# Kernel tuning notes

Hardware: AMD Instinct MI355X
Metric: run time of the kernel (lower is better)

Reference implementation:

```python
import jax, jax.numpy as jnp
import numpy as np

N = 2708
IN_C = 1433
OUT_C = 64


def setup_inputs() -> dict:
    key = jax.random.key(0)
    k1, k2, k3, k4, k5, k6, k7 = jax.random.split(key, 7)
    X = jax.random.normal(k1, (N, IN_C), dtype=jnp.float32)
    A = jax.random.randint(k2, (N, N), 0, 2, dtype=jnp.int32)  # dense binary adjacency mask
    # Graph Fourier basis: orthonormal-ish random matrix (QR of gaussian)
    U = jnp.linalg.qr(jax.random.normal(k3, (N, N), dtype=jnp.float32))[0]
    s = 1.0 / np.sqrt(IN_C)
    W_K = jax.random.normal(k4, (OUT_C, IN_C), dtype=jnp.float32) * s
    W_Q = jax.random.normal(k5, (OUT_C, IN_C), dtype=jnp.float32) * s
    W_V = jax.random.normal(k6, (OUT_C, IN_C), dtype=jnp.float32) * s
    lmbd = jax.random.uniform(k7, (N, 1), dtype=jnp.float32)
    return {"X": X, "A": A, "U": U, "W_K": W_K, "W_Q": W_Q, "W_V": W_V, "lmbd": lmbd}


def reference(X, A, U, W_K, W_Q, W_V, lmbd):
    # Linear projections (torch nn.Linear: x @ W.T)
    K = X @ W_K.T  # [N, d]
    Q = X @ W_Q.T  # [N, d]
    V = X @ W_V.T  # [N, d]
    d_k = K.shape[-1]
    E = (Q @ K.T) / d_k  # [N, N]
    # spectral filtering: igft(lmbd * gft(E)) = U @ (lmbd * (U^T @ E))
    E = jnp.abs(U @ (lmbd * (U.T @ E)))
    # masked softmax over neighbors; dropout p=0 in eval mode (no-op)
    E_masked = jnp.where(A == 0, -jnp.inf, E)
    alpha = jax.nn.softmax(E_masked, axis=-1)
    H = alpha @ V  # [N, d]
    return H
```

## Files before the change

kernel.cpp:

```cpp
#include <hip/hip_runtime.h>

#define NV 2708
#define INC 1433
#define XCOLS 1472
#define UDIM 2752
#define PSTR 2720
#define BSTR 2752
#define SLAB ((size_t)(2752*64))
#define MWPR 88

typedef __attribute__((ext_vector_type(8))) short bf16x8;
typedef __attribute__((ext_vector_type(4))) float f32x4;
typedef __attribute__((ext_vector_type(4))) unsigned short u16x4;

__device__ __forceinline__ unsigned short f2bf(float f){
  union { float f; unsigned int i; } v; v.f = f;
  return (unsigned short)((v.i + 0x7fffu + ((v.i >> 16) & 1u)) >> 16);
}

__global__ __launch_bounds__(256) void convert_pad(
    const float* __restrict__ X, const float* __restrict__ WK,
    const float* __restrict__ WQ, const float* __restrict__ WV,
    const float* __restrict__ U, const int* __restrict__ A,
    unsigned short* __restrict__ Xbf, unsigned short* __restrict__ Wbf,
    unsigned short* __restrict__ Ubf, unsigned int* __restrict__ Abits)
{
  const int wave = threadIdx.x >> 6, lane = threadIdx.x & 63;
  const int row = blockIdx.x*4 + wave;
  const int y = blockIdx.y;
  if (y == 0){
    unsigned short* dst = Ubf + (size_t)row*UDIM;
    if (row < NV){
      const float* src = U + (size_t)row*NV;
      for (int c4 = lane; c4 < UDIM/4; c4 += 64){
        float4 v = make_float4(0.f,0.f,0.f,0.f);
        if (c4 < NV/4) v = *(const float4*)(src + c4*4);
        u16x4 h = { f2bf(v.x), f2bf(v.y), f2bf(v.z), f2bf(v.w) };
        *(u16x4*)(dst + c4*4) = h;
      }
    } else {
      u16x4 zz = {0,0,0,0};
      for (int c4 = lane; c4 < UDIM/4; c4 += 64) *(u16x4*)(dst + c4*4) = zz;
    }
  } else if (y == 1){
    unsigned short* dst = Xbf + (size_t)row*XCOLS;
    if (row < NV){
      const float* src = X + (size_t)row*INC;
      for (int c = lane; c < XCOLS; c += 64)
        dst[c] = (c < INC) ? f2bf(src[c]) : (unsigned short)0;
    } else {
      for (int c = lane; c < XCOLS; c += 64) dst[c] = 0;
    }
  } else if (y == 2){
    if (row >= 192) return;
    const float* s = (row < 64) ? WK : (row < 128) ? WQ : WV;
    const float* src = s + (size_t)(row & 63)*INC;
    unsigned short* dst = Wbf + (size_t)row*XCOLS;
    for (int c = lane; c < XCOLS; c += 64)
      dst[c] = (c < INC) ? f2bf(src[c]) : (unsigned short)0;
  } else {
    if (row >= NV) return;
    const int* arow = A + (size_t)row*NV;
    unsigned int* drow = Abits + (size_t)row*MWPR;
    if (lane < 2) drow[86 + lane] = 0u;
    for (int g = 0; g < 43; g++){
      int j = g*64 + lane;
      int a = (j < NV) ? arow[j] : 0;
      unsigned long long m = __ballot(a != 0);
      if (lane == 0){
        drow[2*g]     = (unsigned int)m;
        drow[2*g + 1] = (unsigned int)(m >> 32);
      }
    }
  }
}

__global__ __launch_bounds__(256) void proj(
    const unsigned short* __restrict__ Xbf, const unsigned short* __restrict__ Wbf,
    float* __restrict__ part)
{
  __shared__ __align__(16) unsigned short At[64*72];
  __shared__ __align__(16) unsigned short Bt[64*72];
  const int tid = threadIdx.x;
  const int lane = tid & 63, wave = tid >> 6, quad = lane >> 4, lr = lane & 15;
  const int m0 = blockIdx.x * 64;
  const int s  = blockIdx.y, z = blockIdx.z;
  const int kbeg = s * 384, kend = min(kbeg + 384, XCOLS);
  const int wm = (wave & 1) * 32, wn = (wave >> 1) * 32;
  const unsigned short* Wz = Wbf + (size_t)z*64*XCOLS;
  const int srow = wave*8 + (lane >> 3), seg = lane & 7;
  f32x4 acc[2][2] = {};

  for (int k0 = kbeg; k0 < kend; k0 += 64){
    #pragma unroll
    for (int e = 0; e < 2; e++){
      int row = e*32 + srow;
      bf16x8 xa = *(const bf16x8*)(Xbf + (size_t)(m0+row)*XCOLS + k0 + seg*8);
      bf16x8 wb = *(const bf16x8*)(Wz  + (size_t)row*XCOLS      + k0 + seg*8);
      *(bf16x8*)&At[row*72 + seg*8] = xa;
      *(bf16x8*)&Bt[row*72 + seg*8] = wb;
    }
    __syncthreads();
    #pragma unroll
    for (int ks = 0; ks < 2; ks++){
      bf16x8 af[2], bv[2];
      #pragma unroll
      for (int t = 0; t < 2; t++){
        af[t] = *(const bf16x8*)&At[(wm + t*16 + lr)*72 + ks*32 + quad*8];
        bv[t] = *(const bf16x8*)&Bt[(wn + t*16 + lr)*72 + ks*32 + quad*8];
      }
      #pragma unroll
      for (int tm = 0; tm < 2; tm++)
        #pragma unroll
        for (int tn = 0; tn < 2; tn++)
          acc[tm][tn] = __builtin_amdgcn_mfma_f32_16x16x32_bf16(af[tm], bv[tn], acc[tm][tn], 0, 0, 0);
    }
    __syncthreads();
  }
  float* dst = part + (size_t)(z*4 + s) * SLAB;
  #pragma unroll
  for (int tm = 0; tm < 2; tm++)
    #pragma unroll
    for (int tn = 0; tn < 2; tn++)
      #pragma unroll
      for (int e = 0; e < 4; e++)
        dst[(size_t)(m0 + wm + tm*16 + quad*4 + e)*64 + wn + tn*16 + lr] = acc[tm][tn][e];
}

__global__ __launch_bounds__(256) void reduce_proj(
    const float* __restrict__ part, unsigned short* __restrict__ K16f,
    unsigned short* __restrict__ QT16, unsigned short* __restrict__ VTf)
{
  int idx = blockIdx.x*256 + threadIdx.x;
  int z = blockIdx.y;
  int m = idx >> 6, c = idx & 63;
  const float* base = part + (size_t)z*4*SLAB + idx;
  float v = 0.f;
  #pragma unroll
  for (int s = 0; s < 4; s++) v += base[s*SLAB];
  unsigned short h = (m < NV) ? f2bf(v) : (unsigned short)0;
  if (z == 0){
    if (m < 2720) K16f[((m>>4)*2 + (c>>5))*512 + (m&15)*32 + (c&31)] = h;
  } else if (z == 1){
    QT16[(size_t)c*BSTR + m] = h;
  } else {
    if (m < 2720) VTf[(m>>5)*2048 + c*32 + (m&31)] = h;
  }
}

__global__ __launch_bounds__(256) void gemmG(
    const unsigned short* __restrict__ Ubf, const unsigned short* __restrict__ QT,
    float* __restrict__ part)
{
  __shared__ __align__(16) unsigned short At[64*72];
  __shared__ __align__(16) unsigned short Bt[64*72];
  const int tid = threadIdx.x;
  const int lane = tid & 63, wave = tid >> 6, quad = lane >> 4, lr = lane & 15;
  const int m0 = blockIdx.x * 64;
  const int s  = blockIdx.y;
  const int kbeg = s * 192, kend = min(kbeg + 192, UDIM);
  const int wm = (wave & 1) * 32, wn = (wave >> 1) * 32;
  const int bc = tid >> 2, bseg = tid & 3;
  const int ml = (lane & 15)*4, koff = wave*16 + (lane >> 4);
  f32x4 acc[2][2] = {};

  for (int k0 = kbeg; k0 < kend; k0 += 64){
    #pragma unroll
    for (int e = 0; e < 4; e++){
      int kl = koff + e*4;
      u16x4 v = *(const u16x4*)(Ubf + (size_t)(k0+kl)*UDIM + m0 + ml);
      At[(ml+0)*72 + kl] = v[0];
      At[(ml+1)*72 + kl] = v[1];
      At[(ml+2)*72 + kl] = v[2];
      At[(ml+3)*72 + kl] = v[3];
    }
    {
      const unsigned short* q = QT + (size_t)bc*BSTR + k0 + bseg*16;
      *(bf16x8*)&Bt[bc*72 + bseg*16]     = *(const bf16x8*)(q);
      *(bf16x8*)&Bt[bc*72 + bseg*16 + 8] = *(const bf16x8*)(q + 8);
    }
    __syncthreads();
    #pragma unroll
    for (int ks = 0; ks < 2; ks++){
      bf16x8 af[2], bv[2];
      #pragma unroll
      for (int t = 0; t < 2; t++){
        af[t] = *(const bf16x8*)&At[(wm + t*16 + lr)*72 + ks*32 + quad*8];
        bv[t] = *(const bf16x8*)&Bt[(wn + t*16 + lr)*72 + ks*32 + quad*8];
      }
      #pragma unroll
      for (int tm = 0; tm < 2; tm++)
        #pragma unroll
        for (int tn = 0; tn < 2; tn++)
          acc[tm][tn] = __builtin_amdgcn_mfma_f32_16x16x32_bf16(af[tm], bv[tn], acc[tm][tn], 0, 0, 0);
    }
    __syncthreads();
  }
  float* dst = part + (size_t)s * SLAB;
  #pragma unroll
  for (int tm = 0; tm < 2; tm++)
    #pragma unroll
    for (int tn = 0; tn < 2; tn++)
      #pragma unroll
      for (int e = 0; e < 4; e++)
        dst[(size_t)(m0 + wm + tm*16 + quad*4 + e)*64 + wn + tn*16 + lr] = acc[tm][tn][e];
}

__global__ __launch_bounds__(256) void reduce_g(
    const float* __restrict__ part, const float* __restrict__ lm,
    unsigned short* __restrict__ G2T)
{
  int idx = blockIdx.x*256 + threadIdx.x;
  int m = idx >> 6, c = idx & 63;
  const float* base = part + idx;
  float v = 0.f;
  #pragma unroll
  for (int s = 0; s < 15; s++) v += base[s*SLAB];
  unsigned short h = 0;
  if (m < NV) h = f2bf(v * lm[m] * (1.0f/64.0f));
  G2T[(size_t)c*BSTR + m] = h;
}

__global__ __launch_bounds__(256) void gemmF(
    const unsigned short* __restrict__ Ubf, const unsigned short* __restrict__ G2T,
    float* __restrict__ part)
{
  __shared__ __align__(16) unsigned short At[64*72];
  __shared__ __align__(16) unsigned short Bt[64*72];
  const int tid = threadIdx.x;
  const int lane = tid & 63, wave = tid >> 6, quad = lane >> 4, lr = lane & 15;
  const int m0 = blockIdx.x * 64;
  const int s  = blockIdx.y;
  const int kbeg = s * 192, kend = min(kbeg + 192, UDIM);
  const int wm = (wave & 1) * 32, wn = (wave >> 1) * 32;
  const int bc = tid >> 2, bseg = tid & 3;
  const int srow = wave*8 + (lane >> 3), seg = lane & 7;
  f32x4 acc[2][2] = {};

  for (int k0 = kbeg; k0 < kend; k0 += 64){
    #pragma unroll
    for (int e = 0; e < 2; e++){
      int row = e*32 + srow;
      bf16x8 ua = *(const bf16x8*)(Ubf + (size_t)(m0+row)*UDIM + k0 + seg*8);
      *(bf16x8*)&At[row*72 + seg*8] = ua;
    }
    {
      const unsigned short* g = G2T + (size_t)bc*BSTR + k0 + bseg*16;
      *(bf16x8*)&Bt[bc*72 + bseg*16]     = *(const bf16x8*)(g);
      *(bf16x8*)&Bt[bc*72 + bseg*16 + 8] = *(const bf16x8*)(g + 8);
    }
    __syncthreads();
    #pragma unroll
    for (int ks = 0; ks < 2; ks++){
      bf16x8 af[2], bv[2];
      #pragma unroll
      for (int t = 0; t < 2; t++){
        af[t] = *(const bf16x8*)&At[(wm + t*16 + lr)*72 + ks*32 + quad*8];
        bv[t] = *(const bf16x8*)&Bt[(wn + t*16 + lr)*72 + ks*32 + quad*8];
      }
      #pragma unroll
      for (int tm = 0; tm < 2; tm++)
        #pragma unroll
        for (int tn = 0; tn < 2; tn++)
          acc[tm][tn] = __builtin_amdgcn_mfma_f32_16x16x32_bf16(af[tm], bv[tn], acc[tm][tn], 0, 0, 0);
    }
    __syncthreads();
  }
  float* dst = part + (size_t)s * SLAB;
  #pragma unroll
  for (int tm = 0; tm < 2; tm++)
    #pragma unroll
    for (int tn = 0; tn < 2; tn++)
      #pragma unroll
      for (int e = 0; e < 4; e++)
        dst[(size_t)(m0 + wm + tm*16 + quad*4 + e)*64 + wn + tn*16 + lr] = acc[tm][tn][e];
}

__global__ __launch_bounds__(256) void reduce_f(
    const float* __restrict__ part, unsigned short* __restrict__ F16)
{
  int idx = blockIdx.x*256 + threadIdx.x;
  int m = idx >> 6;
  const float* base = part + idx;
  float v = 0.f;
  #pragma unroll
  for (int s = 0; s < 15; s++) v += base[s*SLAB];
  F16[idx] = (m < NV) ? f2bf(v) : (unsigned short)0;
}

__global__ __launch_bounds__(256) void fused_attn(
    const unsigned short* __restrict__ F16, const unsigned short* __restrict__ K16f,
    const unsigned int* __restrict__ Abits, const unsigned short* __restrict__ VTf,
    float* __restrict__ Hout)
{
  __shared__ __align__(16) unsigned short pbuf[4*PSTR];
  __shared__ unsigned int mrow[4*MWPR];
  __shared__ float swave[4][4];
  __shared__ float rinv[4];
  const int tid  = threadIdx.x;
  const int lane = tid & 63, wave = tid >> 6;
  const int quad = lane >> 4, lr = lane & 15;
  const int i0 = blockIdx.x * 4;

  for (int idx = tid; idx < 4*MWPR; idx += 256)
    mrow[idx] = Abits[(size_t)i0*MWPR + idx];
  __syncthreads();

  const unsigned short* frow = F16 + (size_t)(i0 + (lr & 3))*64;
  bf16x8 af0 = *(const bf16x8*)(frow + quad*8);
  bf16x8 af1 = *(const bf16x8*)(frow + 32 + quad*8);
  float psum[4] = {0.f, 0.f, 0.f, 0.f};
  for (int t = wave; t < 170; t += 4){
    const unsigned short* kb = K16f + t*1024 + lr*32 + quad*8;
    bf16x8 b0 = *(const bf16x8*)(kb);
    bf16x8 b1 = *(const bf16x8*)(kb + 512);
    f32x4 sv = {};
    sv = __builtin_amdgcn_mfma_f32_16x16x32_bf16(af0, b0, sv, 0, 0, 0);
    sv = __builtin_amdgcn_mfma_f32_16x16x32_bf16(af1, b1, sv, 0, 0, 0);
    if (quad == 0){
      int col = t*16 + lr;
      int wsh = col >> 5, bit = col & 31;
      #pragma unroll
      for (int r = 0; r < 4; r++){
        float p = 0.f;
        if ((mrow[r*MWPR + wsh] >> bit) & 1u) p = __expf(fabsf(sv[r]));
        psum[r] += p;
        pbuf[r*PSTR + col] = f2bf(p);
      }
    }
  }
  #pragma unroll
  for (int r = 0; r < 4; r++){
    float v = psum[r];
    #pragma unroll
    for (int o = 32; o; o >>= 1) v += __shfl_xor(v, o, 64);
    if (lane == 0) swave[wave][r] = v;
  }
  __syncthreads();
  if (tid < 4){
    float sum = swave[0][tid] + swave[1][tid] + swave[2][tid] + swave[3][tid];
    rinv[tid] = (sum > 0.f) ? (1.f/sum) : 0.f;
  }
  __syncthreads();

  const int c0 = wave * 16;
  const int mr = lr & 3;
  f32x4 acc = {};
  for (int kt = 0; kt < 85; kt++){
    bf16x8 af = *(const bf16x8*)&pbuf[mr*PSTR + kt*32 + quad*8];
    bf16x8 bv = *(const bf16x8*)&VTf[kt*2048 + (c0 + lr)*32 + quad*8];
    acc = __builtin_amdgcn_mfma_f32_16x16x32_bf16(af, bv, acc, 0, 0, 0);
  }
  if (quad == 0){
    #pragma unroll
    for (int e = 0; e < 4; e++)
      Hout[(size_t)(i0+e)*64 + c0 + lr] = acc[e] * rinv[e];
  }
}

extern "C" void kernel_launch(void* const* d_in, const int* in_sizes, int n_in,
                              void* d_out, int out_size, void* d_ws, size_t ws_size,
                              hipStream_t stream){
  (void)in_sizes; (void)n_in; (void)out_size; (void)ws_size;
  const float* X  = (const float*)d_in[0];
  const int*   A  = (const int*)d_in[1];
  const float* U  = (const float*)d_in[2];
  const float* WK = (const float*)d_in[3];
  const float* WQ = (const float*)d_in[4];
  const float* WV = (const float*)d_in[5];
  const float* lm = (const float*)d_in[6];

  char* ws = (char*)d_ws;
  size_t off = 0;
  auto alloc = [&](size_t bytes){ size_t o = off; off = (off + bytes + 255) & ~(size_t)255; return o; };
  float*          part = (float*)(ws + alloc(15*SLAB*4));
  unsigned short* Ubf  = (unsigned short*)(ws + alloc((size_t)UDIM*UDIM*2));
  unsigned short* Xbf  = (unsigned short*)(ws + alloc((size_t)UDIM*XCOLS*2));
  unsigned short* Wbf  = (unsigned short*)(ws + alloc((size_t)192*XCOLS*2));
  unsigned short* K16f = (unsigned short*)(ws + alloc((size_t)170*1024*2));
  unsigned short* QT16 = (unsigned short*)(ws + alloc((size_t)64*BSTR*2));
  unsigned short* G2T  = (unsigned short*)(ws + alloc((size_t)64*BSTR*2));
  unsigned short* VTf  = (unsigned short*)(ws + alloc((size_t)85*2048*2));
  unsigned short* F16  = (unsigned short*)(ws + alloc((size_t)2720*64*2));
  unsigned int*   Abits= (unsigned int*)(ws + alloc((size_t)NV*MWPR*4));

  convert_pad<<<dim3(688, 4), 256, 0, stream>>>(X, WK, WQ, WV, U, A, Xbf, Wbf, Ubf, Abits);
  proj<<<dim3(43, 4, 3), 256, 0, stream>>>(Xbf, Wbf, part);
  reduce_proj<<<dim3(688, 3), 256, 0, stream>>>(part, K16f, QT16, VTf);
  gemmG<<<dim3(43, 15), 256, 0, stream>>>(Ubf, QT16, part);
  reduce_g<<<dim3(688), 256, 0, stream>>>(part, lm, G2T);
  gemmF<<<dim3(43, 15), 256, 0, stream>>>(Ubf, G2T, part);
  reduce_f<<<dim3(680), 256, 0, stream>>>(part, F16);
  fused_attn<<<dim3(NV/4), 256, 0, stream>>>(F16, K16f, Abits, VTf, (float*)d_out);
}
```

Before: 213.3 us.

## Process eight query rows per attention block and flatten conversion grid

The fused attention kernel now handles 8 rows per block instead of 4, filling two of the four quads of each 16-row MFMA tile. Each K tile load and V tile load is therefore shared by twice as many rows, and the grid is halved. The conversion kernel is reorganised into a flat 1D grid with one block per row for U, X, and W, and one block per A row split across its four waves. The trade-offs are double the LDS used for the probability buffer and bounds checks on the last, partial row group.

```diff
diff --git a/kernel.cpp b/kernel.cpp
--- a/kernel.cpp
+++ b/kernel.cpp
@@ -18,52 +18,54 @@
   return (unsigned short)((v.i + 0x7fffu + ((v.i >> 16) & 1u)) >> 16);
 }
 
-__global__ __launch_bounds__(256) void convert_pad(
+__global__ __launch_bounds__(256) void convert_all(
     const float* __restrict__ X, const float* __restrict__ WK,
     const float* __restrict__ WQ, const float* __restrict__ WV,
     const float* __restrict__ U, const int* __restrict__ A,
     unsigned short* __restrict__ Xbf, unsigned short* __restrict__ Wbf,
     unsigned short* __restrict__ Ubf, unsigned int* __restrict__ Abits)
 {
-  const int wave = threadIdx.x >> 6, lane = threadIdx.x & 63;
-  const int row = blockIdx.x*4 + wave;
-  const int y = blockIdx.y;
-  if (y == 0){
+  const int bx = blockIdx.x;
+  const int tid = threadIdx.x;
+  if (bx < 2752){
+    const int row = bx;
     unsigned short* dst = Ubf + (size_t)row*UDIM;
     if (row < NV){
       const float* src = U + (size_t)row*NV;
-      for (int c4 = lane; c4 < UDIM/4; c4 += 64){
+      for (int c4 = tid; c4 < 688; c4 += 256){
         float4 v = make_float4(0.f,0.f,0.f,0.f);
-        if (c4 < NV/4) v = *(const float4*)(src + c4*4);
+        if (c4 < 677) v = *(const float4*)(src + c4*4);
         u16x4 h = { f2bf(v.x), f2bf(v.y), f2bf(v.z), f2bf(v.w) };
         *(u16x4*)(dst + c4*4) = h;
       }
     } else {
       u16x4 zz = {0,0,0,0};
-      for (int c4 = lane; c4 < UDIM/4; c4 += 64) *(u16x4*)(dst + c4*4) = zz;
-    }
-  } else if (y == 1){
+      for (int c4 = tid; c4 < 688; c4 += 256) *(u16x4*)(dst + c4*4) = zz;
+    }
+  } else if (bx < 5504){
+    const int row = bx - 2752;
     unsigned short* dst = Xbf + (size_t)row*XCOLS;
     if (row < NV){
       const float* src = X + (size_t)row*INC;
-      for (int c = lane; c < XCOLS; c += 64)
+      for (int c = tid; c < XCOLS; c += 256)
         dst[c] = (c < INC) ? f2bf(src[c]) : (unsigned short)0;
     } else {
-      for (int c = lane; c < XCOLS; c += 64) dst[c] = 0;
-    }
-  } else if (y == 2){
-    if (row >= 192) return;
+      for (int c = tid; c < XCOLS; c += 256) dst[c] = 0;
+    }
+  } else if (bx < 5696){
+    const int row = bx - 5504;
     const float* s = (row < 64) ? WK : (row < 128) ? WQ : WV;
     const float* src = s + (size_t)(row & 63)*INC;
     unsigned short* dst = Wbf + (size_t)row*XCOLS;
-    for (int c = lane; c < XCOLS; c += 64)
+    for (int c = tid; c < XCOLS; c += 256)
       dst[c] = (c < INC) ? f2bf(src[c]) : (unsigned short)0;
   } else {
-    if (row >= NV) return;
-    const int* arow = A + (size_t)row*NV;
-    unsigned int* drow = Abits + (size_t)row*MWPR;
-    if (lane < 2) drow[86 + lane] = 0u;
-    for (int g = 0; g < 43; g++){
+    const int i = bx - 5696;
+    const int lane = tid & 63, wave = tid >> 6;
+    const int* arow = A + (size_t)i*NV;
+    unsigned int* drow = Abits + (size_t)i*MWPR;
+    if (tid < 2) drow[86 + tid] = 0u;
+    for (int g = wave; g < 43; g += 4){
       int j = g*64 + lane;
       int a = (j < NV) ? arow[j] : 0;
       unsigned long long m = __ballot(a != 0);
@@ -293,20 +295,24 @@
     const unsigned int* __restrict__ Abits, const unsigned short* __restrict__ VTf,
     float* __restrict__ Hout)
 {
-  __shared__ __align__(16) unsigned short pbuf[4*PSTR];
-  __shared__ unsigned int mrow[4*MWPR];
-  __shared__ float swave[4][4];
-  __shared__ float rinv[4];
+  __shared__ __align__(16) unsigned short pbuf[8*PSTR];
+  __shared__ unsigned int mrow[8*MWPR];
+  __shared__ float swave[4][8];
+  __shared__ float rinv[8];
   const int tid  = threadIdx.x;
   const int lane = tid & 63, wave = tid >> 6;
   const int quad = lane >> 4, lr = lane & 15;
-  const int i0 = blockIdx.x * 4;
-
-  for (int idx = tid; idx < 4*MWPR; idx += 256)
-    mrow[idx] = Abits[(size_t)i0*MWPR + idx];
+  const int i0 = blockIdx.x * 8;
+
+  for (int idx = tid; idx < 8*MWPR; idx += 256){
+    int r = idx / MWPR;
+    unsigned int v = 0;
+    if (i0 + r < NV) v = Abits[(size_t)(i0 + r)*MWPR + (idx - r*MWPR)];
+    mrow[idx] = v;
+  }
   __syncthreads();
 
-  const unsigned short* frow = F16 + (size_t)(i0 + (lr & 3))*64;
+  const unsigned short* frow = F16 + (size_t)(i0 + (lr & 7))*64;
   bf16x8 af0 = *(const bf16x8*)(frow + quad*8);
   bf16x8 af1 = *(const bf16x8*)(frow + 32 + quad*8);
   float psum[4] = {0.f, 0.f, 0.f, 0.f};
@@ -317,44 +323,48 @@
     f32x4 sv = {};
     sv = __builtin_amdgcn_mfma_f32_16x16x32_bf16(af0, b0, sv, 0, 0, 0);
     sv = __builtin_amdgcn_mfma_f32_16x16x32_bf16(af1, b1, sv, 0, 0, 0);
-    if (quad == 0){
+    if (quad < 2){
       int col = t*16 + lr;
       int wsh = col >> 5, bit = col & 31;
       #pragma unroll
-      for (int r = 0; r < 4; r++){
+      for (int e = 0; e < 4; e++){
+        int r = quad*4 + e;
         float p = 0.f;
-        if ((mrow[r*MWPR + wsh] >> bit) & 1u) p = __expf(fabsf(sv[r]));
-        psum[r] += p;
+        if ((mrow[r*MWPR + wsh] >> bit) & 1u) p = __expf(fabsf(sv[e]));
+        psum[e] += p;
         pbuf[r*PSTR + col] = f2bf(p);
       }
     }
   }
   #pragma unroll
-  for (int r = 0; r < 4; r++){
-    float v = psum[r];
-    #pragma unroll
-    for (int o = 32; o; o >>= 1) v += __shfl_xor(v, o, 64);
-    if (lane == 0) swave[wave][r] = v;
+  for (int e = 0; e < 4; e++){
+    float v = psum[e];
+    #pragma unroll
+    for (int o = 1; o <= 8; o <<= 1) v += __shfl_xor(v, o, 64);
+    if (lr == 0 && quad < 2) swave[wave][quad*4 + e] = v;
   }
   __syncthreads();
-  if (tid < 4){
+  if (tid < 8){
     float sum = swave[0][tid] + swave[1][tid] + swave[2][tid] + swave[3][tid];
     rinv[tid] = (sum > 0.f) ? (1.f/sum) : 0.f;
   }
   __syncthreads();
 
   const int c0 = wave * 16;
-  const int mr = lr & 3;
+  const int mr = lr & 7;
   f32x4 acc = {};
   for (int kt = 0; kt < 85; kt++){
     bf16x8 af = *(const bf16x8*)&pbuf[mr*PSTR + kt*32 + quad*8];
     bf16x8 bv = *(const bf16x8*)&VTf[kt*2048 + (c0 + lr)*32 + quad*8];
     acc = __builtin_amdgcn_mfma_f32_16x16x32_bf16(af, bv, acc, 0, 0, 0);
   }
-  if (quad == 0){
-    #pragma unroll
-    for (int e = 0; e < 4; e++)
-      Hout[(size_t)(i0+e)*64 + c0 + lr] = acc[e] * rinv[e];
+  if (quad < 2){
+    #pragma unroll
+    for (int e = 0; e < 4; e++){
+      int r = quad*4 + e;
+      int i = i0 + r;
+      if (i < NV) Hout[(size_t)i*64 + c0 + lr] = acc[e] * rinv[r];
+    }
   }
 }
 
@@ -384,12 +394,12 @@
   unsigned short* F16  = (unsigned short*)(ws + alloc((size_t)2720*64*2));
   unsigned int*   Abits= (unsigned int*)(ws + alloc((size_t)NV*MWPR*4));
 
-  convert_pad<<<dim3(688, 4), 256, 0, stream>>>(X, WK, WQ, WV, U, A, Xbf, Wbf, Ubf, Abits);
+  convert_all<<<dim3(8404), 256, 0, stream>>>(X, WK, WQ, WV, U, A, Xbf, Wbf, Ubf, Abits);
   proj<<<dim3(43, 4, 3), 256, 0, stream>>>(Xbf, Wbf, part);
   reduce_proj<<<dim3(688, 3), 256, 0, stream>>>(part, K16f, QT16, VTf);
   gemmG<<<dim3(43, 15), 256, 0, stream>>>(Ubf, QT16, part);
   reduce_g<<<dim3(688), 256, 0, stream>>>(part, lm, G2T);
   gemmF<<<dim3(43, 15), 256, 0, stream>>>(Ubf, G2T, part);
   reduce_f<<<dim3(680), 256, 0, stream>>>(part, F16);
-  fused_attn<<<dim3(NV/4), 256, 0, stream>>>(F16, K16f, Abits, VTf, (float*)d_out);
-}
+  fused_attn<<<dim3((NV + 7)/8), 256, 0, stream>>>(F16, K16f, Abits, VTf, (float*)d_out);
+}
```

Result: faster. 197.8 us (-7.2%).
